# Optimization experiments

Measured on AMD Instinct MI355X. Metric: run time of the kernel, lower is better.

The kernel has to match this reference:

```python
import jax, jax.numpy as jnp
import numpy as np

NEG_SLOPE = 0.2  # GATv2Conv default negative_slope
EPS = 1e-5       # BatchNorm1d default eps


def _bn(x, g, b):
    # training-mode batch norm (biased variance, matching torch normalization)
    m = x.mean(0)
    v = x.var(0)
    return (x - m) / jnp.sqrt(v + EPS) * g + b


def setup_inputs() -> dict:
    key = jax.random.key(0)
    N, E, AIN, EIN, HID, H, OUT = 50000, 400000, 64, 16, 64, 8, 1
    ks = jax.random.split(key, 16)
    def nrm(k, shape, s=0.05):
        return jax.random.normal(k, shape, jnp.float32) * s
    return dict(
        x=nrm(ks[0], (N, AIN), 1.0),
        edge_index=jax.random.randint(ks[1], (2, E), 0, N),
        edge_attr=nrm(ks[2], (E, EIN), 1.0),
        W_ap=nrm(ks[3], (AIN, HID)), b_ap=jnp.zeros((HID,), jnp.float32),
        W_ep=nrm(ks[4], (EIN, HID)), b_ep=jnp.zeros((HID,), jnp.float32),
        W_msg=nrm(ks[5], (HID, HID)), b_msg=jnp.zeros((HID,), jnp.float32),
        g_msg=jnp.ones((HID,), jnp.float32), be_msg=jnp.zeros((HID,), jnp.float32),
        W_l=nrm(ks[6], (2 * HID, H * HID)), W_r=nrm(ks[7], (2 * HID, H * HID)),
        att=nrm(ks[8], (H, HID)), b_gat=jnp.zeros((H * HID,), jnp.float32),
        g_bn=jnp.ones((H * HID,), jnp.float32), be_bn=jnp.zeros((H * HID,), jnp.float32),
        W_p1=nrm(ks[9], (H * HID, HID)), b_p1=jnp.zeros((HID,), jnp.float32),
        g_p=jnp.ones((HID,), jnp.float32), be_p=jnp.zeros((HID,), jnp.float32),
        W_p2=nrm(ks[10], (HID, OUT)), b_p2=jnp.zeros((OUT,), jnp.float32),
    )


def reference(x, edge_index, edge_attr,
              W_ap, b_ap, W_ep, b_ep, W_msg, b_msg, g_msg, be_msg,
              W_l, W_r, att, b_gat, g_bn, be_bn,
              W_p1, b_p1, g_p, be_p, W_p2, b_p2):
    N = x.shape[0]
    H, C = att.shape
    row, col = edge_index[0], edge_index[1]

    atom = x @ W_ap + b_ap                      # [N, HID]
    ef = edge_attr @ W_ep + b_ep                # [E, HID]

    # scatter_mean of edge features onto destination nodes
    s = jax.ops.segment_sum(ef, col, num_segments=N)
    cnt = jax.ops.segment_sum(jnp.ones((ef.shape[0],), ef.dtype), col, num_segments=N)
    agg = s / jnp.clip(cnt, 1.0)[:, None]       # [N, HID]

    msg = jax.nn.relu(_bn((atom + agg) @ W_msg + b_msg, g_msg, be_msg))
    comb = jnp.concatenate([msg, agg], axis=1)  # [N, 2*HID]

    # GATv2Conv with default add_self_loops=True, concat=True
    src = jnp.concatenate([row, jnp.arange(N, dtype=row.dtype)])
    dst = jnp.concatenate([col, jnp.arange(N, dtype=col.dtype)])
    xl = (comb @ W_l).reshape(N, H, C)          # source transform
    xr = (comb @ W_r).reshape(N, H, C)          # target transform
    e = jax.nn.leaky_relu(xl[src] + xr[dst], NEG_SLOPE)   # [E+N, H, C]
    score = jnp.einsum('ehc,hc->eh', e, att)               # [E+N, H]
    smax = jax.ops.segment_max(score, dst, num_segments=N)
    ex = jnp.exp(score - smax[dst])
    denom = jax.ops.segment_sum(ex, dst, num_segments=N)
    alpha = ex / denom[dst]                                 # per-dst softmax
    out = jax.ops.segment_sum(alpha[:, :, None] * xl[src], dst, num_segments=N)
    out = out.reshape(N, H * C) + b_gat                     # [N, H*C]

    out = jax.nn.relu(_bn(out, g_bn, be_bn))
    h = jax.nn.relu(_bn(out @ W_p1 + b_p1, g_p, be_p))
    return (h @ W_p2 + b_p2).squeeze(-1)                    # [N]
```

## Files before the change

### kernel.cpp

```cpp
#include <hip/hip_runtime.h>
#include <hip/hip_bf16.h>


#define CDIV(a, b) (((a) + (b) - 1) / (b))

using f32x4 = __attribute__((ext_vector_type(4))) float;
using s16x8 = __attribute__((ext_vector_type(8))) short;
using u32x4 = __attribute__((ext_vector_type(4))) unsigned;

__device__ inline unsigned short f2bf(float f) {
    union { float f; unsigned u; } v; v.f = f;
    unsigned r = v.u + 0x7fff + ((v.u >> 16) & 1);
    return (unsigned short)(r >> 16);
}
__device__ inline float bf_lo(unsigned w) {
    union { unsigned u; float f; } v; v.u = w << 16; return v.f;
}
__device__ inline float bf_hi(unsigned w) {
    union { unsigned u; float f; } v; v.u = w & 0xffff0000u; return v.f;
}
__device__ inline void unp8(u32x4 u, float* v) {
    v[0] = bf_lo(u.x); v[1] = bf_hi(u.x); v[2] = bf_lo(u.y); v[3] = bf_hi(u.y);
    v[4] = bf_lo(u.z); v[5] = bf_hi(u.z); v[6] = bf_lo(u.w); v[7] = bf_hi(u.w);
}

__global__ void k_count(const int* __restrict__ ei, int* __restrict__ cntI, int E) {
    int e = blockIdx.x * blockDim.x + threadIdx.x;
    if (e >= E) return;
    atomicAdd(&cntI[ei[E + e]], 1);
}

__global__ void k_prep(const float* __restrict__ Wl, const float* __restrict__ Wr,
                       const float* __restrict__ Wp1, const float* __restrict__ Wap,
                       const float* __restrict__ Wmsg, const float* __restrict__ bap,
                       const float* __restrict__ bmsg, unsigned short* __restrict__ Wt,
                       unsigned short* __restrict__ Wp1t, unsigned short* __restrict__ Wzt,
                       float* __restrict__ bc) {
    int b = blockIdx.x, t = threadIdx.x;
    if (b < 512) {
        int idx = b * 256 + t;
        int c = idx >> 7, k = idx & 127;
        float v = (c < 512) ? Wl[(size_t)k * 512 + c] : Wr[(size_t)k * 512 + (c - 512)];
        Wt[idx] = f2bf(v);
    } else if (b < 640) {
        int idx = (b - 512) * 256 + t;
        int c = idx >> 9, k = idx & 511;
        Wp1t[idx] = f2bf(Wp1[(size_t)k * 64 + c]);
    } else {
        for (int e = t; e < 4096; e += 256) {
            int i = e >> 6, c = e & 63;
            float s = 0.f;
            for (int j = 0; j < 64; ++j) s += Wap[i * 64 + j] * Wmsg[j * 64 + c];
            Wzt[c * 128 + i] = f2bf(s);
        }
        for (int e = t; e < 4096; e += 256) {
            int k = e >> 6, c = e & 63;
            Wzt[c * 128 + 64 + k] = f2bf(Wmsg[k * 64 + c]);
        }
        if (t < 64) {
            float s = bmsg[t];
            for (int j = 0; j < 64; ++j) s += bap[j] * Wmsg[j * 64 + t];
            bc[t] = s;
        }
    }
}

__global__ void k_bsum(const int* __restrict__ cntI, int* __restrict__ bsum, int N) {
    int b = blockIdx.x, t = threadIdx.x;
    int base = b * 1024 + t * 4;
    int s = 0;
#pragma unroll
    for (int j = 0; j < 4; ++j) { int i = base + j; if (i < N) s += cntI[i]; }
    for (int off = 32; off; off >>= 1) s += __shfl_xor(s, off, 64);
    __shared__ int wsum[4];
    if ((t & 63) == 0) wsum[t >> 6] = s;
    __syncthreads();
    if (t == 0) bsum[b] = wsum[0] + wsum[1] + wsum[2] + wsum[3];
}
__global__ void k_boff(const int* __restrict__ bsum, int* __restrict__ boff, int nb) {
    int t = threadIdx.x;
    if (t < nb) { int s = 0; for (int j = 0; j < t; ++j) s += bsum[j]; boff[t] = s; }
}
__global__ void k_scan2(const int* __restrict__ cntI, const int* __restrict__ boff,
                        int* __restrict__ rowptr, int N) {
    int b = blockIdx.x, t = threadIdx.x;
    int base = b * 1024 + t * 4;
    int v[4]; int s = 0;
#pragma unroll
    for (int j = 0; j < 4; ++j) { int i = base + j; v[j] = (i < N) ? cntI[i] : 0; s += v[j]; }
    __shared__ int ls[256];
    ls[t] = s; __syncthreads();
    for (int off = 1; off < 256; off <<= 1) {
        int tv = (t >= (int)off) ? ls[t - off] : 0;
        __syncthreads(); ls[t] += tv; __syncthreads();
    }
    int run = ls[t] - s + boff[b];
#pragma unroll
    for (int j = 0; j < 4; ++j) { run += v[j]; int i = base + j; if (i < N) rowptr[i + 1] = run; }
    if (b == 0 && t == 0) rowptr[0] = 0;
}

__global__ void k_fill(const int* __restrict__ ei, const int* __restrict__ rowptr,
                       int* __restrict__ cursor, int* __restrict__ esrc,
                       int* __restrict__ eidx, int E) {
    int e = blockIdx.x * blockDim.x + threadIdx.x;
    if (e >= E) return;
    int dst = ei[E + e];
    int pos = rowptr[dst] + atomicAdd(&cursor[dst], 1);
    esrc[pos] = ei[e];
    eidx[pos] = e;
}

__global__ void k_combin(const float* __restrict__ x, const float* __restrict__ ea,
                         const int* __restrict__ rowptr, const int* __restrict__ eidx,
                         const float* __restrict__ Wep, const float* __restrict__ bep,
                         unsigned* __restrict__ combin32, int N) {
    int wid = (blockIdx.x * blockDim.x + threadIdx.x) >> 6;
    int lane = threadIdx.x & 63;
    if (wid >= N) return;
    int e0 = rowptr[wid], e1 = rowptr[wid + 1];
    int deg = e1 - e0;
    int le = lane >> 4, ch = lane & 15;
    float part = 0.f;
    for (int p = e0 + le; p < e1; p += 4)
        part += ea[(size_t)eidx[p] * 16 + ch];
    part += __shfl_xor(part, 16, 64);
    part += __shfl_xor(part, 32, 64);
    float mval = (deg > 0) ? part / (float)deg : 0.f;
    float aggv = bep[lane];
#pragma unroll
    for (int j = 0; j < 16; ++j) {
        float mj = __shfl(mval, j, 64);
        aggv = fmaf(mj, Wep[j * 64 + lane], aggv);
    }
    if (deg == 0) aggv = 0.f;
    float xv = x[(size_t)wid * 64 + lane];
    int i0 = (lane & 31) * 2;
    float ax = __shfl(xv, i0, 64);
    float bx = __shfl(xv, i0 + 1, 64);
    float aa = __shfl(aggv, i0, 64);
    float ba = __shfl(aggv, i0 + 1, 64);
    float a = (lane < 32) ? ax : aa;
    float b = (lane < 32) ? bx : ba;
    combin32[(size_t)wid * 64 + lane] = (unsigned)f2bf(a) | ((unsigned)f2bf(b) << 16);
}

__global__ __launch_bounds__(256) void k_z(
    const unsigned short* __restrict__ combin, const unsigned short* __restrict__ Wzt,
    const float* __restrict__ bc, float* __restrict__ z, float* __restrict__ sums, int N) {
    __shared__ unsigned short a_lds[64 * 128];
    __shared__ unsigned short b_lds[64 * 128];
    __shared__ float redS[64], redQ[64];
    int t = threadIdx.x;
    int row0 = blockIdx.x * 64;
    for (int i = t; i < 1024; i += 256) {
        int row = i >> 4, seg = i & 15;
        int dsts = (row * 256 + ((seg * 16) ^ ((row & 7) << 4))) >> 1;
        int gr = row0 + row;
        s16x8 v = (s16x8)0;
        if (gr < N) v = *(const s16x8*)(combin + (size_t)gr * 128 + seg * 8);
        *(s16x8*)(a_lds + dsts) = v;
        *(s16x8*)(b_lds + dsts) = *(const s16x8*)(Wzt + (size_t)row * 128 + seg * 8);
    }
    if (t < 64) { redS[t] = 0.f; redQ[t] = 0.f; }
    __syncthreads();
    int w = t >> 6, l = t & 63, hi = l >> 4, lo = l & 15;
    int ar = w * 16 + lo;
    s16x8 a[4];
#pragma unroll
    for (int kk = 0; kk < 4; ++kk) {
        int byte = (kk * 64 + hi * 16) ^ ((ar & 7) << 4);
        a[kk] = *(const s16x8*)(a_lds + ((ar * 256 + byte) >> 1));
    }
#pragma unroll
    for (int cf = 0; cf < 4; ++cf) {
        int br = cf * 16 + lo;
        f32x4 acc = (f32x4){0.f, 0.f, 0.f, 0.f};
#pragma unroll
        for (int kk = 0; kk < 4; ++kk) {
            int byte = (kk * 64 + hi * 16) ^ ((br & 7) << 4);
            s16x8 b = *(const s16x8*)(b_lds + ((br * 256 + byte) >> 1));
            acc = __builtin_amdgcn_mfma_f32_16x16x32_bf16(a[kk], b, acc, 0, 0, 0);
        }
        int colg = cf * 16 + lo;
        float bcv = bc[colg];
        float sv = 0.f, qv = 0.f;
#pragma unroll
        for (int r = 0; r < 4; ++r) {
            int rowg = row0 + w * 16 + hi * 4 + r;
            if (rowg < N) {
                float v = acc[r] + bcv;
                z[(size_t)rowg * 64 + colg] = v;
                sv += v; qv += v * v;
            }
        }
        atomicAdd(&redS[colg], sv);
        atomicAdd(&redQ[colg], qv);
    }
    __syncthreads();
    if (t < 64) {
        atomicAdd(&sums[t], redS[t]);
        atomicAdd(&sums[64 + t], redQ[t]);
    }
}

__global__ __launch_bounds__(256) void k_statsg(const u32x4* __restrict__ X,
                                                float* __restrict__ sums, int N) {
    __shared__ float redS[512], redQ[512];
    int t = threadIdx.x;
    for (int i = t; i < 512; i += 256) { redS[i] = 0.f; redQ[i] = 0.f; }
    __syncthreads();
    int qu = t & 63;
    int slice = (blockIdx.x << 2) | (t >> 6);
    int nsl = gridDim.x << 2;
    float s[8], q[8];
#pragma unroll
    for (int j = 0; j < 8; ++j) { s[j] = 0.f; q[j] = 0.f; }
    for (int n = slice; n < N; n += nsl) {
        u32x4 u = X[(size_t)n * 64 + qu];
        unsigned uu[4] = {u.x, u.y, u.z, u.w};
#pragma unroll
        for (int k2 = 0; k2 < 4; ++k2) {
            float a = bf_lo(uu[k2]), b = bf_hi(uu[k2]);
            s[2 * k2] += a; q[2 * k2] += a * a;
            s[2 * k2 + 1] += b; q[2 * k2 + 1] += b * b;
        }
    }
#pragma unroll
    for (int j = 0; j < 8; ++j) {
        atomicAdd(&redS[qu * 8 + j], s[j]);
        atomicAdd(&redQ[qu * 8 + j], q[j]);
    }
    __syncthreads();
    for (int i = t; i < 512; i += 256) {
        atomicAdd(&sums[i], redS[i]);
        atomicAdd(&sums[512 + i], redQ[i]);
    }
}

__global__ void k_comb2(const float* __restrict__ z, const float* __restrict__ sums,
                        const float* __restrict__ g, const float* __restrict__ be,
                        unsigned* __restrict__ combin32, int N) {
    int idx = blockIdx.x * blockDim.x + threadIdx.x;
    if (idx >= N * 16) return;
    int n = idx >> 4, kq = idx & 15;
    float invN = 1.0f / (float)N;
    float4 zv = *(const float4*)(z + (size_t)n * 64 + kq * 4);
    float zz[4] = {zv.x, zv.y, zv.z, zv.w};
    unsigned h[2];
#pragma unroll
    for (int p = 0; p < 2; ++p) {
        unsigned short w[2];
#pragma unroll
        for (int j = 0; j < 2; ++j) {
            int k = kq * 4 + p * 2 + j;
            float mean = sums[k] * invN;
            float var = sums[64 + k] * invN - mean * mean;
            float s = g[k] * rsqrtf(var + 1e-5f);
            float v = fmaxf(fmaf(zz[p * 2 + j], s, be[k] - mean * s), 0.f);
            w[j] = f2bf(v);
        }
        h[p] = (unsigned)w[0] | ((unsigned)w[1] << 16);
    }
    *(uint2*)(combin32 + (size_t)n * 64 + kq * 2) = make_uint2(h[0], h[1]);
}

__global__ __launch_bounds__(256) void k_xlxr2(
    const unsigned short* __restrict__ combin, const unsigned short* __restrict__ Wt,
    unsigned short* __restrict__ xlr, int N) {
    __shared__ unsigned short a_lds[64 * 128];
    __shared__ unsigned short b_lds[256 * 128];
    int t = threadIdx.x;
    int row0 = blockIdx.x * 64;
    int c0 = blockIdx.y * 256;
    for (int i = t; i < 1024; i += 256) {
        int row = i >> 4, seg = i & 15;
        int dsts = (row * 256 + ((seg * 16) ^ ((row & 7) << 4))) >> 1;
        int gr = row0 + row;
        s16x8 v = (s16x8)0;
        if (gr < N) v = *(const s16x8*)(combin + (size_t)gr * 128 + seg * 8);
        *(s16x8*)(a_lds + dsts) = v;
    }
    for (int i = t; i < 4096; i += 256) {
        int row = i >> 4, seg = i & 15;
        int dsts = (row * 256 + ((seg * 16) ^ ((row & 7) << 4))) >> 1;
        *(s16x8*)(b_lds + dsts) = *(const s16x8*)(Wt + (size_t)(c0 + row) * 128 + seg * 8);
    }
    __syncthreads();
    int w = t >> 6, l = t & 63, hi = l >> 4, lo = l & 15;
    int ar = w * 16 + lo;
    s16x8 a[4];
#pragma unroll
    for (int kk = 0; kk < 4; ++kk) {
        int byte = (kk * 64 + hi * 16) ^ ((ar & 7) << 4);
        a[kk] = *(const s16x8*)(a_lds + ((ar * 256 + byte) >> 1));
    }
#pragma unroll
    for (int cf = 0; cf < 16; ++cf) {
        int br = cf * 16 + lo;
        f32x4 acc = (f32x4){0.f, 0.f, 0.f, 0.f};
#pragma unroll
        for (int kk = 0; kk < 4; ++kk) {
            int byte = (kk * 64 + hi * 16) ^ ((br & 7) << 4);
            s16x8 b = *(const s16x8*)(b_lds + ((br * 256 + byte) >> 1));
            acc = __builtin_amdgcn_mfma_f32_16x16x32_bf16(a[kk], b, acc, 0, 0, 0);
        }
        int colg = c0 + cf * 16 + lo;
#pragma unroll
        for (int r = 0; r < 4; ++r) {
            int rowg = row0 + w * 16 + hi * 4 + r;
            if (rowg < N) xlr[(size_t)rowg * 1024 + colg] = f2bf(acc[r]);
        }
    }
}

__device__ inline void gat_edge(u32x4 u, const float* xrv, const float* av,
                                float* acc, float& s) {
    float xlv[8];
    unp8(u, xlv);
    float ps = 0.f;
#pragma unroll
    for (int j = 0; j < 8; ++j) {
        float t = xlv[j] + xrv[j];
        t = fmaxf(t, 0.2f * t);
        ps = fmaf(t, av[j], ps);
    }
    ps += __shfl_xor(ps, 1, 64);
    ps += __shfl_xor(ps, 2, 64);
    ps += __shfl_xor(ps, 4, 64);
    float w = __expf(ps);
    s += w;
#pragma unroll
    for (int j = 0; j < 8; ++j) acc[j] = fmaf(w, xlv[j], acc[j]);
}

__global__ __launch_bounds__(256) void k_gat(
    const unsigned short* __restrict__ xlr, unsigned* __restrict__ gout32,
    const int* __restrict__ rowptr, const int* __restrict__ esrc,
    const float* __restrict__ att, const float* __restrict__ bg, int N) {
    int wid = (blockIdx.x * blockDim.x + threadIdx.x) >> 6;
    int lane = threadIdx.x & 63;
    if (wid >= N) return;
    int n = wid;
    float xrv[8], av[8], acc[8];
    {
        u32x4 u = *(const u32x4*)(xlr + (size_t)n * 1024 + 512 + lane * 8);
        unp8(u, xrv);
    }
    {
        float4 a0 = *(const float4*)(att + lane * 8);
        float4 a1 = *(const float4*)(att + lane * 8 + 4);
        av[0] = a0.x; av[1] = a0.y; av[2] = a0.z; av[3] = a0.w;
        av[4] = a1.x; av[5] = a1.y; av[6] = a1.z; av[7] = a1.w;
    }
#pragma unroll
    for (int j = 0; j < 8; ++j) acc[j] = 0.f;
    float s = 0.f;
    int e0 = rowptr[n], e1 = rowptr[n + 1];
    int m = e1 - e0 + 1;
    for (int base = 0; base < m; base += 64) {
        int ie = e0 + base + lane;
        int myIdx = (ie < e1) ? esrc[ie] : n;
        int cnt = min(64, m - base);
        int i = 0;
        for (; i + 4 <= cnt; i += 4) {
            int s0 = __shfl(myIdx, i, 64);
            int s1 = __shfl(myIdx, i + 1, 64);
            int s2 = __shfl(myIdx, i + 2, 64);
            int s3 = __shfl(myIdx, i + 3, 64);
            u32x4 u0 = *(const u32x4*)(xlr + (size_t)s0 * 1024 + lane * 8);
            u32x4 u1 = *(const u32x4*)(xlr + (size_t)s1 * 1024 + lane * 8);
            u32x4 u2 = *(const u32x4*)(xlr + (size_t)s2 * 1024 + lane * 8);
            u32x4 u3 = *(const u32x4*)(xlr + (size_t)s3 * 1024 + lane * 8);
            gat_edge(u0, xrv, av, acc, s);
            gat_edge(u1, xrv, av, acc, s);
            gat_edge(u2, xrv, av, acc, s);
            gat_edge(u3, xrv, av, acc, s);
        }
        for (; i + 2 <= cnt; i += 2) {
            int s0 = __shfl(myIdx, i, 64);
            int s1 = __shfl(myIdx, i + 1, 64);
            u32x4 u0 = *(const u32x4*)(xlr + (size_t)s0 * 1024 + lane * 8);
            u32x4 u1 = *(const u32x4*)(xlr + (size_t)s1 * 1024 + lane * 8);
            gat_edge(u0, xrv, av, acc, s);
            gat_edge(u1, xrv, av, acc, s);
        }
        if (i < cnt) {
            int s0 = __shfl(myIdx, i, 64);
            u32x4 u0 = *(const u32x4*)(xlr + (size_t)s0 * 1024 + lane * 8);
            gat_edge(u0, xrv, av, acc, s);
        }
    }
    float invs = 1.0f / s;
    float bgv[8];
    {
        float4 b0 = *(const float4*)(bg + lane * 8);
        float4 b1 = *(const float4*)(bg + lane * 8 + 4);
        bgv[0] = b0.x; bgv[1] = b0.y; bgv[2] = b0.z; bgv[3] = b0.w;
        bgv[4] = b1.x; bgv[5] = b1.y; bgv[6] = b1.z; bgv[7] = b1.w;
    }
    u32x4 o;
    o.x = (unsigned)f2bf(acc[0] * invs + bgv[0]) | ((unsigned)f2bf(acc[1] * invs + bgv[1]) << 16);
    o.y = (unsigned)f2bf(acc[2] * invs + bgv[2]) | ((unsigned)f2bf(acc[3] * invs + bgv[3]) << 16);
    o.z = (unsigned)f2bf(acc[4] * invs + bgv[4]) | ((unsigned)f2bf(acc[5] * invs + bgv[5]) << 16);
    o.w = (unsigned)f2bf(acc[6] * invs + bgv[6]) | ((unsigned)f2bf(acc[7] * invs + bgv[7]) << 16);
    *(u32x4*)(gout32 + (size_t)n * 256 + lane * 4) = o;
}

__global__ __launch_bounds__(256) void k_postm(
    const unsigned* __restrict__ gout32, const unsigned short* __restrict__ Wp1t,
    const float* __restrict__ gsums, const float* __restrict__ g,
    const float* __restrict__ be, const float* __restrict__ bp1,
    float* __restrict__ h1, float* __restrict__ sums, int N) {
    __shared__ unsigned short a_lds[64 * 128];
    __shared__ unsigned short b_lds[64 * 128];
    __shared__ float sc_l[512], sh_l[512];
    __shared__ float redS[64], redQ[64];
    int t = threadIdx.x;
    float invN = 1.0f / (float)N;
    for (int i = t; i < 512; i += 256) {
        float mean = gsums[i] * invN;
        float var = gsums[512 + i] * invN - mean * mean;
        float s = g[i] * rsqrtf(var + 1e-5f);
        sc_l[i] = s;
        sh_l[i] = be[i] - mean * s;
    }
    if (t < 64) { redS[t] = 0.f; redQ[t] = 0.f; }
    int row0 = blockIdx.x * 64;
    int w = t >> 6, l = t & 63, hi = l >> 4, lo = l & 15;
    int ar = w * 16 + lo;
    f32x4 acc[4];
#pragma unroll
    for (int cf = 0; cf < 4; ++cf) acc[cf] = (f32x4){0.f, 0.f, 0.f, 0.f};
    for (int kc = 0; kc < 4; ++kc) {
        __syncthreads();
        for (int i = t; i < 1024; i += 256) {
            int row = i >> 4, seg = i & 15;
            int dsts = (row * 256 + ((seg * 16) ^ ((row & 7) << 4))) >> 1;
            int gr = row0 + row;
            int k0 = kc * 128 + seg * 8;
            s16x8 v = (s16x8)0;
            if (gr < N) {
                u32x4 u = *(const u32x4*)(gout32 + (size_t)gr * 256 + (k0 >> 1));
                float f[8];
                unp8(u, f);
#pragma unroll
                for (int j = 0; j < 8; ++j) {
                    float y = fmaxf(fmaf(f[j], sc_l[k0 + j], sh_l[k0 + j]), 0.f);
                    v[j] = (short)f2bf(y);
                }
            }
            *(s16x8*)(a_lds + dsts) = v;
            *(s16x8*)(b_lds + dsts) = *(const s16x8*)(Wp1t + (size_t)row * 512 + k0);
        }
        __syncthreads();
        s16x8 a[4];
#pragma unroll
        for (int kk = 0; kk < 4; ++kk) {
            int byte = (kk * 64 + hi * 16) ^ ((ar & 7) << 4);
            a[kk] = *(const s16x8*)(a_lds + ((ar * 256 + byte) >> 1));
        }
#pragma unroll
        for (int cf = 0; cf < 4; ++cf) {
            int br = cf * 16 + lo;
#pragma unroll
            for (int kk = 0; kk < 4; ++kk) {
                int byte = (kk * 64 + hi * 16) ^ ((br & 7) << 4);
                s16x8 b = *(const s16x8*)(b_lds + ((br * 256 + byte) >> 1));
                acc[cf] = __builtin_amdgcn_mfma_f32_16x16x32_bf16(a[kk], b, acc[cf], 0, 0, 0);
            }
        }
    }
#pragma unroll
    for (int cf = 0; cf < 4; ++cf) {
        int colg = cf * 16 + lo;
        float bv = bp1[colg];
        float sv = 0.f, qv = 0.f;
#pragma unroll
        for (int r = 0; r < 4; ++r) {
            int rowg = row0 + w * 16 + hi * 4 + r;
            if (rowg < N) {
                float v = acc[cf][r] + bv;
                h1[(size_t)rowg * 64 + colg] = v;
                sv += v; qv += v * v;
            }
        }
        atomicAdd(&redS[colg], sv);
        atomicAdd(&redQ[colg], qv);
    }
    __syncthreads();
    if (t < 64) {
        atomicAdd(&sums[t], redS[t]);
        atomicAdd(&sums[64 + t], redQ[t]);
    }
}

__global__ void k_final(const float* __restrict__ h1, const float* __restrict__ stats,
                        const float* __restrict__ g, const float* __restrict__ be,
                        const float* __restrict__ Wp2, const float* __restrict__ bp2,
                        float* __restrict__ out, int N) {
    int wid = (blockIdx.x * blockDim.x + threadIdx.x) >> 6;
    int lane = threadIdx.x & 63;
    if (wid >= N) return;
    float invN = 1.0f / (float)N;
    float mean = stats[lane] * invN;
    float var = stats[64 + lane] * invN - mean * mean;
    float inv = rsqrtf(var + 1e-5f);
    float v = h1[(size_t)wid * 64 + lane];
    v = fmaxf((v - mean) * (inv * g[lane]) + be[lane], 0.f);
    float p = v * Wp2[lane];
#pragma unroll
    for (int off = 32; off; off >>= 1) p += __shfl_xor(p, off, 64);
    if (lane == 0) out[wid] = p + bp2[0];
}

extern "C" void kernel_launch(void* const* d_in, const int* in_sizes, int n_in,
                              void* d_out, int out_size, void* d_ws, size_t ws_size,
                              hipStream_t stream) {
    const float* x      = (const float*)d_in[0];
    const int*   ei     = (const int*)d_in[1];
    const float* ea     = (const float*)d_in[2];
    const float* W_ap   = (const float*)d_in[3];
    const float* b_ap   = (const float*)d_in[4];
    const float* W_ep   = (const float*)d_in[5];
    const float* b_ep   = (const float*)d_in[6];
    const float* W_msg  = (const float*)d_in[7];
    const float* b_msg  = (const float*)d_in[8];
    const float* g_msg  = (const float*)d_in[9];
    const float* be_msg = (const float*)d_in[10];
    const float* W_l    = (const float*)d_in[11];
    const float* W_r    = (const float*)d_in[12];
    const float* att    = (const float*)d_in[13];
    const float* b_gat  = (const float*)d_in[14];
    const float* g_bn   = (const float*)d_in[15];
    const float* be_bn  = (const float*)d_in[16];
    const float* W_p1   = (const float*)d_in[17];
    const float* b_p1   = (const float*)d_in[18];
    const float* g_p    = (const float*)d_in[19];
    const float* be_p   = (const float*)d_in[20];
    const float* W_p2   = (const float*)d_in[21];
    const float* b_p2   = (const float*)d_in[22];

    int N = in_sizes[0] / 64;
    int E = in_sizes[1] / 2;
    int nb = CDIV(N, 1024);

    float* ws = (float*)d_ws;
    size_t off = 0;
    int*   cntI   = (int*)(ws + off); off += N;
    int*   cursor = (int*)(ws + off); off += N;
    float* st_msg = ws + off; off += 128;
    float* st_gat = ws + off; off += 1024;
    float* st_p   = ws + off; off += 128;
    size_t zero_floats = off;
    unsigned short* combin = (unsigned short*)(ws + off); off += (size_t)N * 64;
    float* zb     = ws + off; off += (size_t)N * 64;
    unsigned short* Wzt = (unsigned short*)(ws + off); off += 4096;
    float* bc     = ws + off; off += 64;
    int*   rowptr = (int*)(ws + off); off += (size_t)(N + 1); off = (off + 3) & ~(size_t)3;
    int*   esrc   = (int*)(ws + off); off += E;
    int*   eidx   = (int*)(ws + off); off += E;
    int*   bsum   = (int*)(ws + off); off += 64;
    int*   boff   = (int*)(ws + off); off += 64;
    unsigned short* Wt  = (unsigned short*)(ws + off); off += 65536;
    unsigned short* Wp1t = (unsigned short*)(ws + off); off += 16384;
    unsigned short* xlr = (unsigned short*)(ws + off); off += (size_t)N * 512;
    unsigned* gout32 = (unsigned*)(ws + off); off += (size_t)N * 256;
    float* h1 = zb;

    hipMemsetAsync(d_ws, 0, zero_floats * sizeof(float), stream);

    k_prep<<<641, 256, 0, stream>>>(W_l, W_r, W_p1, W_ap, W_msg, b_ap, b_msg,
                                    Wt, Wp1t, Wzt, bc);
    k_count<<<CDIV(E, 256), 256, 0, stream>>>(ei, cntI, E);
    k_bsum<<<nb, 256, 0, stream>>>(cntI, bsum, N);
    k_boff<<<1, 64, 0, stream>>>(bsum, boff, nb);
    k_scan2<<<nb, 256, 0, stream>>>(cntI, boff, rowptr, N);
    k_fill<<<CDIV(E, 256), 256, 0, stream>>>(ei, rowptr, cursor, esrc, eidx, E);
    k_combin<<<CDIV(N * 64, 256), 256, 0, stream>>>(x, ea, rowptr, eidx, W_ep, b_ep,
                                                    (unsigned*)combin, N);
    k_z<<<CDIV(N, 64), 256, 0, stream>>>(combin, Wzt, bc, zb, st_msg, N);
    k_comb2<<<CDIV(N * 16, 256), 256, 0, stream>>>(zb, st_msg, g_msg, be_msg,
                                                   (unsigned*)combin, N);
    dim3 gx(CDIV(N, 64), 4);
    k_xlxr2<<<gx, 256, 0, stream>>>(combin, Wt, xlr, N);
    k_gat<<<CDIV(N * 64, 256), 256, 0, stream>>>(xlr, gout32, rowptr, esrc, att, b_gat, N);
    k_statsg<<<256, 256, 0, stream>>>((const u32x4*)gout32, st_gat, N);
    k_postm<<<CDIV(N, 64), 256, 0, stream>>>(gout32, Wp1t, st_gat, g_bn, be_bn,
                                             b_p1, h1, st_p, N);
    k_final<<<CDIV(N * 64, 256), 256, 0, stream>>>(h1, st_p, g_p, be_p, W_p2, b_p2,
                                                   (float*)d_out, N);
}
```

Before: 384.2 us.

## Schedule GAT node waves by in-degree and fuse edge counting into prep kernel

```diff
diff --git a/kernel.cpp b/kernel.cpp
--- a/kernel.cpp
+++ b/kernel.cpp
@@ -24,18 +24,13 @@
     v[4] = bf_lo(u.z); v[5] = bf_hi(u.z); v[6] = bf_lo(u.w); v[7] = bf_hi(u.w);
 }
 
-__global__ void k_count(const int* __restrict__ ei, int* __restrict__ cntI, int E) {
-    int e = blockIdx.x * blockDim.x + threadIdx.x;
-    if (e >= E) return;
-    atomicAdd(&cntI[ei[E + e]], 1);
-}
-
-__global__ void k_prep(const float* __restrict__ Wl, const float* __restrict__ Wr,
-                       const float* __restrict__ Wp1, const float* __restrict__ Wap,
-                       const float* __restrict__ Wmsg, const float* __restrict__ bap,
-                       const float* __restrict__ bmsg, unsigned short* __restrict__ Wt,
-                       unsigned short* __restrict__ Wp1t, unsigned short* __restrict__ Wzt,
-                       float* __restrict__ bc) {
+__global__ void k_prepcnt(const float* __restrict__ Wl, const float* __restrict__ Wr,
+                          const float* __restrict__ Wp1, const float* __restrict__ Wap,
+                          const float* __restrict__ Wmsg, const float* __restrict__ bap,
+                          const float* __restrict__ bmsg, unsigned short* __restrict__ Wt,
+                          unsigned short* __restrict__ Wp1t, unsigned short* __restrict__ Wzt,
+                          float* __restrict__ bc, const int* __restrict__ ei,
+                          int* __restrict__ cntI, int E) {
     int b = blockIdx.x, t = threadIdx.x;
     if (b < 512) {
         int idx = b * 256 + t;
@@ -46,7 +41,7 @@
         int idx = (b - 512) * 256 + t;
         int c = idx >> 9, k = idx & 511;
         Wp1t[idx] = f2bf(Wp1[(size_t)k * 64 + c]);
-    } else {
+    } else if (b == 640) {
         for (int e = t; e < 4096; e += 256) {
             int i = e >> 6, c = e & 63;
             float s = 0.f;
@@ -62,6 +57,9 @@
             for (int j = 0; j < 64; ++j) s += bap[j] * Wmsg[j * 64 + t];
             bc[t] = s;
         }
+    } else {
+        int e = (b - 641) * 256 + t;
+        if (e < E) atomicAdd(&cntI[ei[E + e]], 1);
     }
 }
 
@@ -98,6 +96,29 @@
 #pragma unroll
     for (int j = 0; j < 4; ++j) { run += v[j]; int i = base + j; if (i < N) rowptr[i + 1] = run; }
     if (b == 0 && t == 0) rowptr[0] = 0;
+}
+
+__global__ void k_dhist(const int* __restrict__ cntI, int* __restrict__ dcnt, int N) {
+    int n = blockIdx.x * blockDim.x + threadIdx.x;
+    if (n >= N) return;
+    atomicAdd(&dcnt[min(cntI[n], 255)], 1);
+}
+__global__ void k_dscan(const int* __restrict__ dcnt, int* __restrict__ dstart) {
+    __shared__ int s[256];
+    int t = threadIdx.x;
+    s[t] = dcnt[t];
+    __syncthreads();
+    int acc = 0;
+    for (int d = t + 1; d < 256; ++d) acc += s[d];
+    dstart[t] = acc;
+}
+__global__ void k_dfill(const int* __restrict__ cntI, const int* __restrict__ dstart,
+                        int* __restrict__ dcur, int* __restrict__ perm, int N) {
+    int n = blockIdx.x * blockDim.x + threadIdx.x;
+    if (n >= N) return;
+    int d = min(cntI[n], 255);
+    int pos = dstart[d] + atomicAdd(&dcur[d], 1);
+    perm[pos] = n;
 }
 
 __global__ void k_fill(const int* __restrict__ ei, const int* __restrict__ rowptr,
@@ -337,11 +358,12 @@
 __global__ __launch_bounds__(256) void k_gat(
     const unsigned short* __restrict__ xlr, unsigned* __restrict__ gout32,
     const int* __restrict__ rowptr, const int* __restrict__ esrc,
-    const float* __restrict__ att, const float* __restrict__ bg, int N) {
+    const int* __restrict__ perm, const float* __restrict__ att,
+    const float* __restrict__ bg, int N) {
     int wid = (blockIdx.x * blockDim.x + threadIdx.x) >> 6;
     int lane = threadIdx.x & 63;
     if (wid >= N) return;
-    int n = wid;
+    int n = perm[wid];
     float xrv[8], av[8], acc[8];
     {
         u32x4 u = *(const u32x4*)(xlr + (size_t)n * 1024 + 512 + lane * 8);
@@ -549,10 +571,14 @@
     size_t off = 0;
     int*   cntI   = (int*)(ws + off); off += N;
     int*   cursor = (int*)(ws + off); off += N;
+    int*   dcnt   = (int*)(ws + off); off += 256;
+    int*   dcur   = (int*)(ws + off); off += 256;
     float* st_msg = ws + off; off += 128;
     float* st_gat = ws + off; off += 1024;
     float* st_p   = ws + off; off += 128;
     size_t zero_floats = off;
+    int*   dstart = (int*)(ws + off); off += 256;
+    int*   perm   = (int*)(ws + off); off += N;
     unsigned short* combin = (unsigned short*)(ws + off); off += (size_t)N * 64;
     float* zb     = ws + off; off += (size_t)N * 64;
     unsigned short* Wzt = (unsigned short*)(ws + off); off += 4096;
@@ -570,12 +596,14 @@
 
     hipMemsetAsync(d_ws, 0, zero_floats * sizeof(float), stream);
 
-    k_prep<<<641, 256, 0, stream>>>(W_l, W_r, W_p1, W_ap, W_msg, b_ap, b_msg,
-                                    Wt, Wp1t, Wzt, bc);
-    k_count<<<CDIV(E, 256), 256, 0, stream>>>(ei, cntI, E);
+    k_prepcnt<<<641 + CDIV(E, 256), 256, 0, stream>>>(
+        W_l, W_r, W_p1, W_ap, W_msg, b_ap, b_msg, Wt, Wp1t, Wzt, bc, ei, cntI, E);
     k_bsum<<<nb, 256, 0, stream>>>(cntI, bsum, N);
     k_boff<<<1, 64, 0, stream>>>(bsum, boff, nb);
     k_scan2<<<nb, 256, 0, stream>>>(cntI, boff, rowptr, N);
+    k_dhist<<<CDIV(N, 256), 256, 0, stream>>>(cntI, dcnt, N);
+    k_dscan<<<1, 256, 0, stream>>>(dcnt, dstart);
+    k_dfill<<<CDIV(N, 256), 256, 0, stream>>>(cntI, dstart, dcur, perm, N);
     k_fill<<<CDIV(E, 256), 256, 0, stream>>>(ei, rowptr, cursor, esrc, eidx, E);
     k_combin<<<CDIV(N * 64, 256), 256, 0, stream>>>(x, ea, rowptr, eidx, W_ep, b_ep,
                                                     (unsigned*)combin, N);
@@ -584,7 +612,8 @@
                                                    (unsigned*)combin, N);
     dim3 gx(CDIV(N, 64), 4);
     k_xlxr2<<<gx, 256, 0, stream>>>(combin, Wt, xlr, N);
-    k_gat<<<CDIV(N * 64, 256), 256, 0, stream>>>(xlr, gout32, rowptr, esrc, att, b_gat, N);
+    k_gat<<<CDIV(N * 64, 256), 256, 0, stream>>>(xlr, gout32, rowptr, esrc, perm,
+                                                 att, b_gat, N);
     k_statsg<<<256, 256, 0, stream>>>((const u32x4*)gout32, st_gat, N);
     k_postm<<<CDIV(N, 64), 256, 0, stream>>>(gout32, Wp1t, st_gat, g_bn, be_bn,
                                              b_p1, h1, st_p, N);
```

Measured after the change: 722.6 us. 1.88x slower.
